# Performance work log

Measured on AMD Instinct MI355X. Metric: run time of the kernel, lower is better.

## Reference

```python
import jax, jax.numpy as jnp
import numpy as np

D_MODEL = 1024
NHEAD = 16
HEAD_DIM = D_MODEL // NHEAD
EPS = 1e-5


def _layer_norm(x, gamma, beta):
    mu = jnp.mean(x, axis=-1, keepdims=True)
    var = jnp.mean(jnp.square(x - mu), axis=-1, keepdims=True)
    return (x - mu) * jax.lax.rsqrt(var + EPS) * gamma + beta


def setup_inputs() -> dict:
    key = jax.random.key(0)
    ks = jax.random.split(key, 8)
    s = 1.0 / np.sqrt(D_MODEL)
    return {
        "x": jax.random.normal(ks[0], (4, 2048, D_MODEL), dtype=jnp.float32),
        "Wq": jax.random.uniform(ks[1], (D_MODEL, D_MODEL), jnp.float32, -s, s),
        "Wk": jax.random.uniform(ks[2], (D_MODEL, D_MODEL), jnp.float32, -s, s),
        "Wv": jax.random.uniform(ks[3], (D_MODEL, D_MODEL), jnp.float32, -s, s),
        "ln1_g": jnp.ones((D_MODEL,), jnp.float32),
        "ln1_b": jnp.zeros((D_MODEL,), jnp.float32),
        "ln2_g": jnp.ones((D_MODEL,), jnp.float32),
        "ln2_b": jnp.zeros((D_MODEL,), jnp.float32),
        "W1": jax.random.uniform(ks[4], (D_MODEL, D_MODEL), jnp.float32, -s, s),
        "b1": jax.random.uniform(ks[5], (D_MODEL,), jnp.float32, -s, s),
        "W2": jax.random.uniform(ks[6], (D_MODEL, D_MODEL), jnp.float32, -s, s),
        "b2": jax.random.uniform(ks[7], (D_MODEL,), jnp.float32, -s, s),
    }


def reference(x, Wq, Wk, Wv, ln1_g, ln1_b, ln2_g, ln2_b, W1, b1, W2, b2):
    B, S, D = x.shape
    temperature = jnp.sqrt(jnp.asarray(D_MODEL / NHEAD, x.dtype))
    xn = _layer_norm(x, ln1_g, ln1_b)
    # torch Linear: y = x @ W.T (weights are [out, in], no bias for q/k/v)
    q = (xn @ Wq.T).reshape(B, S, NHEAD, HEAD_DIM)
    k = (xn @ Wk.T).reshape(B, S, NHEAD, HEAD_DIM)
    v = (xn @ Wv.T).reshape(B, S, NHEAD, HEAD_DIM)
    scores = jnp.einsum("bqhd,bkhd->bhqk", q, k) / temperature  # [B,H,S,S]
    causal = jnp.tril(jnp.ones((S, S), dtype=bool))
    scores = jnp.where(causal, scores, jnp.asarray(-jnp.inf, scores.dtype))
    attn = jax.nn.softmax(scores, axis=-1)
    att_out = jnp.einsum("bhqk,bkhd->bqhd", attn, v).reshape(B, S, D)
    xt = x + att_out
    xt2 = _layer_norm(xt, ln2_g, ln2_b)
    ffn = jax.nn.relu(xt2 @ W1.T + b1) @ W2.T + b2  # dropout=0 -> identity
    return xt + ffn
```

## Files before the change

kernel.cpp:

```cpp
#include <hip/hip_runtime.h>
#include <hip/hip_bf16.h>

typedef unsigned short u16;
typedef unsigned int u32;
typedef __attribute__((ext_vector_type(8))) __bf16 bf16x8;
typedef __attribute__((ext_vector_type(4))) float f32x4;
typedef __attribute__((ext_vector_type(8))) unsigned short ushort8v;
typedef __attribute__((ext_vector_type(4))) unsigned short u16x4;
typedef __attribute__((ext_vector_type(2))) unsigned int u32x2;

#define DEV __device__ __forceinline__

DEV u16 f2bf(float f) {
    union { float f; unsigned int i; } u; u.f = f;
    unsigned int x = u.i;
    unsigned int r = (x + 0x7fffu + ((x >> 16) & 1u)) >> 16;
    return (u16)r;
}
DEV float bf2f(u16 h) {
    union { unsigned int i; float f; } u; u.i = ((unsigned int)h) << 16;
    return u.f;
}
DEV u32 cvt_pk_bf16(float lo, float hi) {
    u32 r;
    asm("v_cvt_pk_bf16_f32 %0, %1, %2" : "=v"(r) : "v"(lo), "v"(hi));
    return r;
}

__global__ __launch_bounds__(256) void cvt_w(
    const float* __restrict__ wq, const float* __restrict__ wk,
    const float* __restrict__ wv, const float* __restrict__ w1,
    const float* __restrict__ w2, u16* __restrict__ dst)
{
    const int i = (blockIdx.x * 256 + threadIdx.x) * 4;
    if (i >= (1 << 20)) return;
    auto conv4 = [](float4 a) {
        u16x4 r; r[0] = f2bf(a.x); r[1] = f2bf(a.y); r[2] = f2bf(a.z); r[3] = f2bf(a.w);
        return r;
    };
    *(u16x4*)(dst + i)               = conv4(*(const float4*)(wq + i));
    *(u16x4*)(dst + (1 << 20) + i)   = conv4(*(const float4*)(wk + i));
    *(u16x4*)(dst + (2 << 20) + i)   = conv4(*(const float4*)(wv + i));
    *(u16x4*)(dst + (3 << 20) + i)   = conv4(*(const float4*)(w1 + i));
    *(u16x4*)(dst + (4 << 20) + i)   = conv4(*(const float4*)(w2 + i));
}

template<bool ADD>
__global__ __launch_bounds__(256) void ln_kernel(
    const float* __restrict__ xin, const u16* __restrict__ addbf,
    const float* __restrict__ g, const float* __restrict__ be,
    float* __restrict__ xt_out, u16* __restrict__ y_bf)
{
    const int row = blockIdx.x;
    const int tid = threadIdx.x;
    const size_t base = (size_t)row * 1024 + tid * 4;

    float4 xv = *(const float4*)(xin + base);
    float v[4] = {xv.x, xv.y, xv.z, xv.w};
    if (ADD) {
        u16x4 a = *(const u16x4*)(addbf + base);
        v[0] += bf2f(a[0]); v[1] += bf2f(a[1]); v[2] += bf2f(a[2]); v[3] += bf2f(a[3]);
        float4 o; o.x = v[0]; o.y = v[1]; o.z = v[2]; o.w = v[3];
        *(float4*)(xt_out + base) = o;
    }
    float s = 0.f, ss = 0.f;
    #pragma unroll
    for (int j = 0; j < 4; ++j) { s += v[j]; ss += v[j] * v[j]; }
    #pragma unroll
    for (int o = 32; o > 0; o >>= 1) { s += __shfl_xor(s, o); ss += __shfl_xor(ss, o); }
    __shared__ float red[8];
    const int w = tid >> 6;
    if ((tid & 63) == 0) { red[w * 2] = s; red[w * 2 + 1] = ss; }
    __syncthreads();
    s  = red[0] + red[2] + red[4] + red[6];
    ss = red[1] + red[3] + red[5] + red[7];
    const float mu = s * (1.0f / 1024.0f);
    const float var = ss * (1.0f / 1024.0f) - mu * mu;
    const float rstd = rsqrtf(var + 1e-5f);

    const int col = tid * 4;
    float4 gv = *(const float4*)(g + col);
    float4 bv = *(const float4*)(be + col);
    u16x4 o4;
    o4[0] = f2bf((v[0] - mu) * rstd * gv.x + bv.x);
    o4[1] = f2bf((v[1] - mu) * rstd * gv.y + bv.y);
    o4[2] = f2bf((v[2] - mu) * rstd * gv.z + bv.z);
    o4[3] = f2bf((v[3] - mu) * rstd * gv.w + bv.w);
    *(u16x4*)(y_bf + base) = o4;
}

template<int EPI>
__global__ __launch_bounds__(256, 2) void gemm_bt(
    const u16* __restrict__ A, const u16* __restrict__ Bt,
    void* __restrict__ Cout, const float* __restrict__ bias,
    const float* __restrict__ resid, int M, int N, int K)
{
    __shared__ u16 As[128 * 32];
    __shared__ u16 Bs[128 * 32];
    const int tid = threadIdx.x;
    const int l = tid & 63;
    const int w = tid >> 6;
    const int wm = w >> 1, wn = w & 1;
    const int fr = l & 15, fc = l >> 4;
    const size_t rowA0 = (size_t)blockIdx.x * 128;
    const size_t rowB0 = (size_t)blockIdx.y * 128;

    f32x4 acc[4][4] = {};
    const int ldoff = fr * 32 + fc * 8;

    const int nkt = K >> 5;
    for (int kt = 0; kt < nkt; ++kt) {
        __syncthreads();
        const int k0 = kt << 5;
        #pragma unroll
        for (int p = 0; p < 2; ++p) {
            const int rr = p * 64 + w * 16 + (l >> 2);
            const int cc = (l & 3) * 8;
            const u16* ga = A  + (rowA0 + rr) * K + k0 + cc;
            const u16* gb = Bt + (rowB0 + rr) * K + k0 + cc;
            __builtin_amdgcn_global_load_lds(
                (const __attribute__((address_space(1))) void*)ga,
                (__attribute__((address_space(3))) void*)(As + (p * 64 + w * 16) * 32),
                16, 0, 0);
            __builtin_amdgcn_global_load_lds(
                (const __attribute__((address_space(1))) void*)gb,
                (__attribute__((address_space(3))) void*)(Bs + (p * 64 + w * 16) * 32),
                16, 0, 0);
        }
        __syncthreads();
        bf16x8 af[4], bfv[4];
        #pragma unroll
        for (int m = 0; m < 4; ++m)
            af[m] = *(const bf16x8*)(As + (wm * 64 + m * 16) * 32 + ldoff);
        #pragma unroll
        for (int n = 0; n < 4; ++n)
            bfv[n] = *(const bf16x8*)(Bs + (wn * 64 + n * 16) * 32 + ldoff);
        #pragma unroll
        for (int m = 0; m < 4; ++m)
            #pragma unroll
            for (int n = 0; n < 4; ++n)
                acc[m][n] = __builtin_amdgcn_mfma_f32_16x16x32_bf16(
                    af[m], bfv[n], acc[m][n], 0, 0, 0);
    }

    const int r0 = (int)rowA0 + wm * 64;
    const int c0 = (int)rowB0 + wn * 64;
    #pragma unroll
    for (int m = 0; m < 4; ++m) {
        #pragma unroll
        for (int n = 0; n < 4; ++n) {
            const int row = r0 + m * 16 + fc * 4;
            const int col = c0 + n * 16 + fr;
            #pragma unroll
            for (int j = 0; j < 4; ++j) {
                float v = acc[m][n][j];
                if constexpr (EPI == 0) {
                    const int rowj = row + j;
                    const int which = col >> 10;
                    const int hh = (col >> 6) & 15;
                    const int dd = col & 63;
                    const size_t dst = (size_t)which * 8388608 +
                        ((((size_t)(rowj >> 11) * 16 + hh) * 2048 + (rowj & 2047)) * 64 + dd);
                    ((u16*)Cout)[dst] = f2bf(v);
                } else if constexpr (EPI == 1) {
                    const size_t idx = (size_t)(row + j) * N + col;
                    v += bias[col];
                    v = fmaxf(v, 0.0f);
                    ((u16*)Cout)[idx] = f2bf(v);
                } else {
                    const size_t idx = (size_t)(row + j) * N + col;
                    v += bias[col] + resid[idx];
                    ((float*)Cout)[idx] = v;
                }
            }
        }
    }
}

__global__ __launch_bounds__(256, 4) void attn_fwd(
    const u16* __restrict__ Qh, const u16* __restrict__ Kh,
    const u16* __restrict__ Vh, u16* __restrict__ attout)
{
    __shared__ u16 Ks[64 * 64];
    __shared__ u16 Vt[64 * 64];
    __shared__ u16 Pw[4 * 16 * 64];

    const int bid = blockIdx.x;
    const int pair = (bid >> 3) & 15;
    const int g = (bid & 7) + 8 * (bid >> 7);
    const int h = g & 15, b = g >> 4;

    const int tid = threadIdx.x, l = tid & 63, w = tid >> 6;
    const int fr = l & 15, fc = l >> 4;
    const int hb = b * 16 + h;
    const size_t head = (size_t)hb << 17;
    const u16* kb_g = Kh + head;
    const u16* vb_g = Vh + head;
    u16* pw = Pw + w * 1024;

    const int sw = (fr & 7) << 3;
    const int col0 = (fc * 8) ^ sw;
    const int col1 = col0 ^ 32;

    const int kr = tid >> 2;
    const int kc0 = (tid & 3) * 16;
    const int kd0 = kc0 ^ ((kr & 7) << 3);
    const int kd1 = (kc0 + 8) ^ ((kr & 7) << 3);

    const float qs = 0.125f * 1.44269504f;

    bf16x8 onesv;
    #pragma unroll
    for (int j = 0; j < 8; ++j) onesv[j] = (__bf16)1.0f;

    #pragma unroll 1
    for (int half = 0; half < 2; ++half) {
        const int qt = half ? 31 - pair : pair;
        const int qbase = qt * 64 + w * 16;
        const int qg = qbase + fr;

        const u16* qp = Qh + head + (size_t)(qbase + fr) * 64 + fc * 8;
        bf16x8 qf0 = *(const bf16x8*)qp;
        bf16x8 qf1 = *(const bf16x8*)(qp + 32);
        #pragma unroll
        for (int j = 0; j < 8; ++j) {
            qf0[j] = (__bf16)((float)qf0[j] * qs);
            qf1[j] = (__bf16)((float)qf1[j] * qs);
        }

        f32x4 acc_o[4] = {};
        float m_run = -3.0e38f;
        float l_run[4] = {0.f, 0.f, 0.f, 0.f};

        const int nkt = qt + 1;
        ushort8v kA = *(const ushort8v*)(kb_g + (size_t)kr * 64 + kc0);
        ushort8v kB = *(const ushort8v*)(kb_g + (size_t)kr * 64 + kc0 + 8);
        ushort8v vA = *(const ushort8v*)(vb_g + (size_t)kr * 64 + kc0);
        ushort8v vB = *(const ushort8v*)(vb_g + (size_t)kr * 64 + kc0 + 8);

        #pragma unroll 1
        for (int kt = 0; kt < nkt; ++kt) {
            const int kv0 = kt * 64;
            const bool diag = (kt == qt);
            __syncthreads();
            *(ushort8v*)(Ks + kr * 64 + kd0) = kA;
            *(ushort8v*)(Ks + kr * 64 + kd1) = kB;
            #pragma unroll
            for (int j = 0; j < 8; ++j) {
                const int d0 = kc0 + j, d1 = kc0 + 8 + j;
                Vt[d0 * 64 + (kr ^ ((d0 & 7) << 3) ^ ((d0 >> 4) << 4))] = vA[j];
                Vt[d1 * 64 + (kr ^ ((d1 & 7) << 3) ^ ((d1 >> 4) << 4))] = vB[j];
            }
            __syncthreads();
            if (kt + 1 < nkt) {
                const u16* kn = kb_g + (size_t)(kv0 + 64 + kr) * 64 + kc0;
                const u16* vn = vb_g + (size_t)(kv0 + 64 + kr) * 64 + kc0;
                kA = *(const ushort8v*)kn; kB = *(const ushort8v*)(kn + 8);
                vA = *(const ushort8v*)vn; vB = *(const ushort8v*)(vn + 8);
            }

            f32x4 sa[4] = {};
            __builtin_amdgcn_s_setprio(1);
            #pragma unroll
            for (int nb = 0; nb < 4; ++nb) {
                const u16* kb = Ks + (nb * 16 + fr) * 64;
                sa[nb] = __builtin_amdgcn_mfma_f32_16x16x32_bf16(
                    *(const bf16x8*)(kb + col0), qf0, sa[nb], 0, 0, 0);
                sa[nb] = __builtin_amdgcn_mfma_f32_16x16x32_bf16(
                    *(const bf16x8*)(kb + col1), qf1, sa[nb], 0, 0, 0);
            }
            __builtin_amdgcn_s_setprio(0);

            if (diag) {
                #pragma unroll
                for (int nb = 0; nb < 4; ++nb)
                    #pragma unroll
                    for (int j = 0; j < 4; ++j) {
                        const int kg = kv0 + nb * 16 + fc * 4 + j;
                        if (kg > qg) sa[nb][j] = -3.0e38f;
                    }
            }

            float mx = sa[0][0];
            #pragma unroll
            for (int nb = 0; nb < 4; ++nb)
                #pragma unroll
                for (int j = 0; j < 4; ++j)
                    mx = fmaxf(mx, sa[nb][j]);
            mx = fmaxf(mx, __shfl_xor(mx, 16));
            mx = fmaxf(mx, __shfl_xor(mx, 32));

            if (__any(mx > m_run + 8.0f)) {
                const float mn = fmaxf(m_run, mx);
                const float alpha = exp2f(m_run - mn);
                m_run = mn;
                float aj[4];
                #pragma unroll
                for (int j = 0; j < 4; ++j)
                    aj[j] = __shfl(alpha, fc * 4 + j);
                #pragma unroll
                for (int j = 0; j < 4; ++j)
                    l_run[j] *= aj[j];
                #pragma unroll
                for (int db = 0; db < 4; ++db)
                    #pragma unroll
                    for (int j = 0; j < 4; ++j)
                        acc_o[db][j] *= aj[j];
            }

            #pragma unroll
            for (int nb = 0; nb < 4; ++nb)
                #pragma unroll
                for (int j = 0; j < 4; ++j)
                    sa[nb][j] = exp2f(sa[nb][j] - m_run);

            #pragma unroll
            for (int nb = 0; nb < 4; ++nb) {
                u32x2 pkv;
                pkv[0] = cvt_pk_bf16(sa[nb][0], sa[nb][1]);
                pkv[1] = cvt_pk_bf16(sa[nb][2], sa[nb][3]);
                *(u32x2*)(pw + fr * 64 + ((nb * 16 + fc * 4) ^ sw)) = pkv;
            }
            const u16* prd = pw + fr * 64;
            const bf16x8 pf0 = *(const bf16x8*)(prd + col0);
            const bf16x8 pf1 = *(const bf16x8*)(prd + col1);
            f32x4 acc_s = {};
            __builtin_amdgcn_s_setprio(1);
            #pragma unroll
            for (int db = 0; db < 4; ++db) {
                const u16* vb = Vt + (db * 16 + fr) * 64;
                const int vx = db << 4;
                acc_o[db] = __builtin_amdgcn_mfma_f32_16x16x32_bf16(
                    pf0, *(const bf16x8*)(vb + (col0 ^ vx)), acc_o[db], 0, 0, 0);
                acc_o[db] = __builtin_amdgcn_mfma_f32_16x16x32_bf16(
                    pf1, *(const bf16x8*)(vb + (col1 ^ vx)), acc_o[db], 0, 0, 0);
            }
            acc_s = __builtin_amdgcn_mfma_f32_16x16x32_bf16(pf0, onesv, acc_s, 0, 0, 0);
            acc_s = __builtin_amdgcn_mfma_f32_16x16x32_bf16(pf1, onesv, acc_s, 0, 0, 0);
            __builtin_amdgcn_s_setprio(0);
            #pragma unroll
            for (int j = 0; j < 4; ++j)
                l_run[j] += acc_s[j];
        }

        float inv[4];
        #pragma unroll
        for (int j = 0; j < 4; ++j) inv[j] = 1.0f / l_run[j];
        const size_t bS = (size_t)b * 2048;
        #pragma unroll
        for (int db = 0; db < 4; ++db)
            #pragma unroll
            for (int j = 0; j < 4; ++j)
                attout[(bS + qbase + fc * 4 + j) * 1024 + h * 64 + db * 16 + fr] =
                    f2bf(acc_o[db][j] * inv[j]);
    }
}

extern "C" void kernel_launch(void* const* d_in, const int* in_sizes, int n_in,
                              void* d_out, int out_size, void* d_ws, size_t ws_size,
                              hipStream_t stream)
{
    const float* x    = (const float*)d_in[0];
    const float* Wq   = (const float*)d_in[1];
    const float* Wk   = (const float*)d_in[2];
    const float* Wv   = (const float*)d_in[3];
    const float* ln1g = (const float*)d_in[4];
    const float* ln1b = (const float*)d_in[5];
    const float* ln2g = (const float*)d_in[6];
    const float* ln2b = (const float*)d_in[7];
    const float* W1   = (const float*)d_in[8];
    const float* b1   = (const float*)d_in[9];
    const float* W2   = (const float*)d_in[10];
    const float* b2   = (const float*)d_in[11];

    char* ws = (char*)d_ws;
    u16*   wbf  = (u16*)(ws);
    u16*   xn   = (u16*)(ws + 10485760);
    u16*   qkvb = (u16*)(ws + 27262976);
    u16*   attb = (u16*)(ws + 77594624);
    float* xt   = (float*)(ws + 94371840);

    cvt_w<<<1024, 256, 0, stream>>>(Wq, Wk, Wv, W1, W2, wbf);
    ln_kernel<false><<<8192, 256, 0, stream>>>(x, nullptr, ln1g, ln1b, nullptr, xn);
    gemm_bt<0><<<dim3(64, 24), 256, 0, stream>>>(xn, wbf, qkvb, nullptr, nullptr,
                                                 8192, 3072, 1024);
    attn_fwd<<<1024, 256, 0, stream>>>(qkvb, qkvb + 8388608, qkvb + 16777216, attb);
    ln_kernel<true><<<8192, 256, 0, stream>>>(x, attb, ln2g, ln2b, xt, xn);
    gemm_bt<1><<<dim3(64, 8), 256, 0, stream>>>(xn, wbf + (3 << 20), qkvb, b1, nullptr,
                                                8192, 1024, 1024);
    gemm_bt<2><<<dim3(64, 8), 256, 0, stream>>>(qkvb, wbf + (4 << 20), d_out, b2, xt,
                                                8192, 1024, 1024);
}
```

Measured before the change: 238.1 us.

## Double-buffer attention K/V tiles with async LDS loads and deepen GEMM k-step

In the attention kernel, K and V tiles are now double-buffered in shared memory. K is loaded straight into LDS with global_load_lds, and V is prefetched two tiles ahead in registers and transposed into the next buffer after the PV MFMAs. This replaces the two barriers per tile with one barrier plus hand-placed waitcnts. The GEMM now loads a 64-wide K slab per iteration, which halves the barrier count and doubles its LDS use, at some risk to occupancy.

```diff
diff --git a/kernel.cpp b/kernel.cpp
--- a/kernel.cpp
+++ b/kernel.cpp
@@ -10,6 +10,8 @@
 typedef __attribute__((ext_vector_type(2))) unsigned int u32x2;
 
 #define DEV __device__ __forceinline__
+#define AS1 __attribute__((address_space(1)))
+#define AS3 __attribute__((address_space(3)))
 
 DEV u16 f2bf(float f) {
     union { float f; unsigned int i; } u; u.f = f;
@@ -95,8 +97,8 @@
     void* __restrict__ Cout, const float* __restrict__ bias,
     const float* __restrict__ resid, int M, int N, int K)
 {
-    __shared__ u16 As[128 * 32];
-    __shared__ u16 Bs[128 * 32];
+    __shared__ u16 As[2 * 128 * 32];
+    __shared__ u16 Bs[2 * 128 * 32];
     const int tid = threadIdx.x;
     const int l = tid & 63;
     const int w = tid >> 6;
@@ -108,39 +110,40 @@
     f32x4 acc[4][4] = {};
     const int ldoff = fr * 32 + fc * 8;
 
-    const int nkt = K >> 5;
+    const int nkt = K >> 6;
     for (int kt = 0; kt < nkt; ++kt) {
         __syncthreads();
-        const int k0 = kt << 5;
-        #pragma unroll
-        for (int p = 0; p < 2; ++p) {
-            const int rr = p * 64 + w * 16 + (l >> 2);
-            const int cc = (l & 3) * 8;
-            const u16* ga = A  + (rowA0 + rr) * K + k0 + cc;
-            const u16* gb = Bt + (rowB0 + rr) * K + k0 + cc;
-            __builtin_amdgcn_global_load_lds(
-                (const __attribute__((address_space(1))) void*)ga,
-                (__attribute__((address_space(3))) void*)(As + (p * 64 + w * 16) * 32),
-                16, 0, 0);
-            __builtin_amdgcn_global_load_lds(
-                (const __attribute__((address_space(1))) void*)gb,
-                (__attribute__((address_space(3))) void*)(Bs + (p * 64 + w * 16) * 32),
-                16, 0, 0);
+        const int k0 = kt << 6;
+        #pragma unroll
+        for (int q = 0; q < 4; ++q) {
+            const int row = (q & 1) * 64 + w * 16 + (l >> 2);
+            const int kk  = (q >> 1) * 32 + (l & 3) * 8;
+            const u16* ga = A  + (rowA0 + row) * K + k0 + kk;
+            const u16* gb = Bt + (rowB0 + row) * K + k0 + kk;
+            u16* da = As + q * 2048 + w * 512;
+            u16* db = Bs + q * 2048 + w * 512;
+            __builtin_amdgcn_global_load_lds((const AS1 void*)ga, (AS3 void*)da, 16, 0, 0);
+            __builtin_amdgcn_global_load_lds((const AS1 void*)gb, (AS3 void*)db, 16, 0, 0);
         }
         __syncthreads();
-        bf16x8 af[4], bfv[4];
-        #pragma unroll
-        for (int m = 0; m < 4; ++m)
-            af[m] = *(const bf16x8*)(As + (wm * 64 + m * 16) * 32 + ldoff);
-        #pragma unroll
-        for (int n = 0; n < 4; ++n)
-            bfv[n] = *(const bf16x8*)(Bs + (wn * 64 + n * 16) * 32 + ldoff);
-        #pragma unroll
-        for (int m = 0; m < 4; ++m)
+        #pragma unroll
+        for (int ks = 0; ks < 2; ++ks) {
+            const u16* as_p = As + ks * 4096;
+            const u16* bs_p = Bs + ks * 4096;
+            bf16x8 af[4], bfv[4];
+            #pragma unroll
+            for (int m = 0; m < 4; ++m)
+                af[m] = *(const bf16x8*)(as_p + (wm * 64 + m * 16) * 32 + ldoff);
             #pragma unroll
             for (int n = 0; n < 4; ++n)
-                acc[m][n] = __builtin_amdgcn_mfma_f32_16x16x32_bf16(
-                    af[m], bfv[n], acc[m][n], 0, 0, 0);
+                bfv[n] = *(const bf16x8*)(bs_p + (wn * 64 + n * 16) * 32 + ldoff);
+            #pragma unroll
+            for (int m = 0; m < 4; ++m)
+                #pragma unroll
+                for (int n = 0; n < 4; ++n)
+                    acc[m][n] = __builtin_amdgcn_mfma_f32_16x16x32_bf16(
+                        af[m], bfv[n], acc[m][n], 0, 0, 0);
+        }
     }
 
     const int r0 = (int)rowA0 + wm * 64;
@@ -181,8 +184,8 @@
     const u16* __restrict__ Qh, const u16* __restrict__ Kh,
     const u16* __restrict__ Vh, u16* __restrict__ attout)
 {
-    __shared__ u16 Ks[64 * 64];
-    __shared__ u16 Vt[64 * 64];
+    __shared__ u16 Ks[2][64 * 64];
+    __shared__ u16 Vt[2][64 * 64];
     __shared__ u16 Pw[4 * 16 * 64];
 
     const int bid = blockIdx.x;
@@ -202,10 +205,11 @@
     const int col0 = (fc * 8) ^ sw;
     const int col1 = col0 ^ 32;
 
+    const int krow0 = w * 16 + (l >> 3);
+    const int kdsw  = ((l & 7) * 8) ^ ((l >> 3) << 3);
+
     const int kr = tid >> 2;
     const int kc0 = (tid & 3) * 16;
-    const int kd0 = kc0 ^ ((kr & 7) << 3);
-    const int kd1 = (kc0 + 8) ^ ((kr & 7) << 3);
 
     const float qs = 0.125f * 1.44269504f;
 
@@ -233,37 +237,61 @@
         float l_run[4] = {0.f, 0.f, 0.f, 0.f};
 
         const int nkt = qt + 1;
-        ushort8v kA = *(const ushort8v*)(kb_g + (size_t)kr * 64 + kc0);
-        ushort8v kB = *(const ushort8v*)(kb_g + (size_t)kr * 64 + kc0 + 8);
-        ushort8v vA = *(const ushort8v*)(vb_g + (size_t)kr * 64 + kc0);
-        ushort8v vB = *(const ushort8v*)(vb_g + (size_t)kr * 64 + kc0 + 8);
+        int cur = 0;
+
+        #pragma unroll
+        for (int i = 0; i < 2; ++i) {
+            const int row = krow0 + i * 8;
+            __builtin_amdgcn_global_load_lds(
+                (const AS1 void*)(kb_g + (size_t)row * 64 + kdsw),
+                (AS3 void*)(&Ks[0][0] + (w * 16 + i * 8) * 64), 16, 0, 0);
+        }
+        __builtin_amdgcn_sched_barrier(0);
+        {
+            ushort8v v0a = *(const ushort8v*)(vb_g + (size_t)kr * 64 + kc0);
+            ushort8v v0b = *(const ushort8v*)(vb_g + (size_t)kr * 64 + kc0 + 8);
+            #pragma unroll
+            for (int j = 0; j < 8; ++j) {
+                const int d0 = kc0 + j, d1 = kc0 + 8 + j;
+                Vt[0][d0 * 64 + (kr ^ ((d0 & 7) << 3) ^ ((d0 >> 4) << 4))] = v0a[j];
+                Vt[0][d1 * 64 + (kr ^ ((d1 & 7) << 3) ^ ((d1 >> 4) << 4))] = v0b[j];
+            }
+        }
+        ushort8v vA, vB;
+        if (nkt > 1) {
+            vA = *(const ushort8v*)(vb_g + (size_t)(64 + kr) * 64 + kc0);
+            vB = *(const ushort8v*)(vb_g + (size_t)(64 + kr) * 64 + kc0 + 8);
+        }
+        __builtin_amdgcn_sched_barrier(0);
+        if (nkt > 1) asm volatile("s_waitcnt vmcnt(2)" ::: "memory");
+        else         asm volatile("s_waitcnt vmcnt(0)" ::: "memory");
+        asm volatile("s_waitcnt lgkmcnt(0)" ::: "memory");
+        __builtin_amdgcn_s_barrier();
 
         #pragma unroll 1
         for (int kt = 0; kt < nkt; ++kt) {
             const int kv0 = kt * 64;
             const bool diag = (kt == qt);
-            __syncthreads();
-            *(ushort8v*)(Ks + kr * 64 + kd0) = kA;
-            *(ushort8v*)(Ks + kr * 64 + kd1) = kB;
-            #pragma unroll
-            for (int j = 0; j < 8; ++j) {
-                const int d0 = kc0 + j, d1 = kc0 + 8 + j;
-                Vt[d0 * 64 + (kr ^ ((d0 & 7) << 3) ^ ((d0 >> 4) << 4))] = vA[j];
-                Vt[d1 * 64 + (kr ^ ((d1 & 7) << 3) ^ ((d1 >> 4) << 4))] = vB[j];
-            }
-            __syncthreads();
+            const u16* ksc = &Ks[cur][0];
+            const u16* vtc = &Vt[cur][0];
+
             if (kt + 1 < nkt) {
-                const u16* kn = kb_g + (size_t)(kv0 + 64 + kr) * 64 + kc0;
-                const u16* vn = vb_g + (size_t)(kv0 + 64 + kr) * 64 + kc0;
-                kA = *(const ushort8v*)kn; kB = *(const ushort8v*)(kn + 8);
-                vA = *(const ushort8v*)vn; vB = *(const ushort8v*)(vn + 8);
-            }
+                u16* ksn = &Ks[cur ^ 1][0];
+                #pragma unroll
+                for (int i = 0; i < 2; ++i) {
+                    const int row = krow0 + i * 8;
+                    __builtin_amdgcn_global_load_lds(
+                        (const AS1 void*)(kb_g + (size_t)(kv0 + 64 + row) * 64 + kdsw),
+                        (AS3 void*)(ksn + (w * 16 + i * 8) * 64), 16, 0, 0);
+                }
+            }
+            __builtin_amdgcn_sched_barrier(0);
 
             f32x4 sa[4] = {};
             __builtin_amdgcn_s_setprio(1);
             #pragma unroll
             for (int nb = 0; nb < 4; ++nb) {
-                const u16* kb = Ks + (nb * 16 + fr) * 64;
+                const u16* kb = ksc + (nb * 16 + fr) * 64;
                 sa[nb] = __builtin_amdgcn_mfma_f32_16x16x32_bf16(
                     *(const bf16x8*)(kb + col0), qf0, sa[nb], 0, 0, 0);
                 sa[nb] = __builtin_amdgcn_mfma_f32_16x16x32_bf16(
@@ -328,7 +356,7 @@
             __builtin_amdgcn_s_setprio(1);
             #pragma unroll
             for (int db = 0; db < 4; ++db) {
-                const u16* vb = Vt + (db * 16 + fr) * 64;
+                const u16* vb = vtc + (db * 16 + fr) * 64;
                 const int vx = db << 4;
                 acc_o[db] = __builtin_amdgcn_mfma_f32_16x16x32_bf16(
                     pf0, *(const bf16x8*)(vb + (col0 ^ vx)), acc_o[db], 0, 0, 0);
@@ -341,6 +369,29 @@
             #pragma unroll
             for (int j = 0; j < 4; ++j)
                 l_run[j] += acc_s[j];
+
+            if (kt + 1 < nkt) {
+                u16* vtn = &Vt[cur ^ 1][0];
+                #pragma unroll
+                for (int j = 0; j < 8; ++j) {
+                    const int d0 = kc0 + j, d1 = kc0 + 8 + j;
+                    vtn[d0 * 64 + (kr ^ ((d0 & 7) << 3) ^ ((d0 >> 4) << 4))] = vA[j];
+                    vtn[d1 * 64 + (kr ^ ((d1 & 7) << 3) ^ ((d1 >> 4) << 4))] = vB[j];
+                }
+            }
+            if (kt + 2 < nkt) {
+                const u16* vn = vb_g + (size_t)(kv0 + 128 + kr) * 64 + kc0;
+                vA = *(const ushort8v*)vn;
+                vB = *(const ushort8v*)(vn + 8);
+            }
+            __builtin_amdgcn_sched_barrier(0);
+            if (kt + 1 < nkt) {
+                if (kt + 2 < nkt) asm volatile("s_waitcnt vmcnt(2)" ::: "memory");
+                else              asm volatile("s_waitcnt vmcnt(0)" ::: "memory");
+            }
+            asm volatile("s_waitcnt lgkmcnt(0)" ::: "memory");
+            __builtin_amdgcn_s_barrier();
+            cur ^= 1;
         }
 
         float inv[4];
```

Result: faster. 227.7 us (-4.3%).
